# Performance work log

Measured on AMD Instinct MI355X. Metric: run time of the kernel, lower is better.

The kernel has to match this reference:

```python
import jax, jax.numpy as jnp
import numpy as np

NUM_HEADS, NUM_KEYS, NUM_VALUES, NUM_OUTPUTS = 8, 64, 64, 512
B, H, W, C = 16, 64, 64, 512


def setup_inputs() -> dict:
    key = jax.random.key(0)
    ks = jax.random.split(key, 5)
    def xavier(k, shape):
        fan_in, fan_out = shape
        lim = np.sqrt(6.0 / (fan_in + fan_out))
        return jax.random.uniform(k, shape, jnp.float32, -lim, lim)
    return {
        "x": jax.random.normal(ks[0], (B, H, W, C), jnp.float32),
        "Wq": xavier(ks[1], (C, NUM_HEADS * NUM_KEYS)),
        "bq": jnp.zeros((NUM_HEADS * NUM_KEYS,), jnp.float32),
        "Wk": xavier(ks[2], (C, NUM_HEADS * NUM_KEYS)),
        "bk": jnp.zeros((NUM_HEADS * NUM_KEYS,), jnp.float32),
        "Wv": xavier(ks[3], (C, NUM_HEADS * NUM_VALUES)),
        "bv": jnp.zeros((NUM_HEADS * NUM_VALUES,), jnp.float32),
        "Wo": xavier(ks[4], (NUM_VALUES, NUM_OUTPUTS)),
        "bo": jnp.zeros((NUM_OUTPUTS,), jnp.float32),
    }


def reference(x, Wq, bq, Wk, bk, Wv, bv, Wo, bo):
    b, h, w, c = x.shape
    n, dk, dv = NUM_HEADS, NUM_KEYS, NUM_VALUES
    # single pooled query per image
    q = (jnp.mean(x, axis=(1, 2)) @ Wq + bq).reshape(b, n, dk)      # [B,N,dk]
    K = (x @ Wk + bk).reshape(b, h, w, n, dk)                        # [B,H,W,N,dk]
    V = (x @ Wv + bv).reshape(b, h, w, n, dv)                        # [B,H,W,N,dv]
    scale = 1.0 / jnp.sqrt(jnp.float32(dk))
    # scores of the single query against every pixel
    s = jnp.einsum('bnk,bhwnk->bnhw', q, K) * scale                  # [B,N,H,W]
    attn_h = jax.nn.softmax(s, axis=-1)   # per row, softmax over width
    attn_v = jax.nn.softmax(s, axis=-2)   # per column, softmax over height
    A_h = jnp.einsum('bnhw,bhwnv->bnhv', attn_h, V)                  # [B,N,H,dv]
    A_v = jnp.einsum('bnhw,bhwnv->bnwv', attn_v, V)                  # [B,N,W,dv]
    # outer-product combine over spatial dims, summed over heads
    A = jnp.einsum('bnhv,bnwv->bhwv', A_h, A_v)                      # [B,H,W,dv]
    return A @ Wo + bo                                               # [B,H,W,num_outputs]
```

## Files before the change

### kernel.cpp

```cpp
#include <hip/hip_runtime.h>
#include <hip/hip_bf16.h>

#define NHEADS 8
#define DK 64
#define DV 64
#define CIN 512
#define PIX_PER_IMG 4096
#define NPIX 65536

typedef short bf16x8 __attribute__((ext_vector_type(8)));
typedef float f32x4 __attribute__((ext_vector_type(4)));

__device__ __forceinline__ float b2f(unsigned int u) {
  union { unsigned int i; float f; } v; v.i = u << 16; return v.f;
}
__device__ __forceinline__ unsigned short f2b(float f) {
  union { float f; unsigned int i; } v; v.f = f;
  unsigned int x = v.i;
  return (unsigned short)((x + 0x7fffu + ((x >> 16) & 1u)) >> 16);
}
__device__ __forceinline__ void gload_lds16(const void* g, void* l) {
  __builtin_amdgcn_global_load_lds(
      (const __attribute__((address_space(1))) void*)g,
      (__attribute__((address_space(3))) void*)l, 16, 0, 0);
}

__global__ __launch_bounds__(256) void k_pool_prep(
    const float* __restrict__ x, unsigned short* __restrict__ xb,
    float* __restrict__ partial,
    const float* __restrict__ Wv, const float* __restrict__ Wo,
    unsigned short* __restrict__ WvT, unsigned short* __restrict__ WoT) {
  int blk = blockIdx.x;
  int t = threadIdx.x;
  if (blk >= 2048) {
    int idx = (blk - 2048) * 256 + t;
    if (idx < 262144) {
      int n = idx >> 9, c = idx & 511;
      WvT[idx] = f2b(Wv[(size_t)c * 512 + n]);
    } else {
      int j = idx - 262144;
      int o = j >> 6, kk = j & 63;
      WoT[j] = f2b(Wo[(size_t)kk * 512 + o]);
    }
    return;
  }
  int b = blk >> 7, chunk = blk & 127;
  int c4 = t & 127;
  int half = t >> 7;
  size_t rowbase = (size_t)b * PIX_PER_IMG + chunk * 32;
  const float4* x4 = (const float4*)x;
  float4 acc = make_float4(0.f, 0.f, 0.f, 0.f);
#pragma unroll
  for (int i = 0; i < 16; ++i) {
    int p = 2 * i + half;
    float4 v = x4[(rowbase + p) * 128 + c4];
    acc.x += v.x; acc.y += v.y; acc.z += v.z; acc.w += v.w;
    uint2 o;
    o.x = (unsigned)f2b(v.x) | ((unsigned)f2b(v.y) << 16);
    o.y = (unsigned)f2b(v.z) | ((unsigned)f2b(v.w) << 16);
    *(uint2*)(xb + (rowbase + p) * CIN + c4 * 4) = o;
  }
  *(float4*)(partial + ((size_t)(blk * 2 + half)) * CIN + c4 * 4) = acc;
}

__global__ __launch_bounds__(256) void k_qp2(
    const float* __restrict__ partial,
    const float* __restrict__ Wq, const float* __restrict__ bq,
    const float* __restrict__ Wk, float* __restrict__ P) {
  __shared__ float xs[CIN];
  __shared__ float red[256];
  __shared__ float qsh[64];
  int b = blockIdx.x, n = blockIdx.y, t = threadIdx.x;
  for (int c = t; c < CIN; c += 256) {
    float s = 0.f;
    for (int ch = 0; ch < 256; ++ch) s += partial[((size_t)(b * 256 + ch)) * CIN + c];
    xs[c] = s * (1.0f / 4096.0f);
  }
  __syncthreads();
  int jj = t & 63, part = t >> 6;
  {
    float acc = 0.f;
    const float* wp = Wq + (size_t)(part * 128) * CIN + n * 64 + jj;
    for (int ci = 0; ci < 128; ++ci)
      acc += xs[part * 128 + ci] * wp[(size_t)ci * CIN];
    red[t] = acc;
  }
  __syncthreads();
  if (t < 64)
    qsh[t] = red[t] + red[t + 64] + red[t + 128] + red[t + 192] + bq[n * 64 + t];
  __syncthreads();
  for (int c = t; c < CIN; c += 256) {
    float acc = 0.f;
    const float* wr = Wk + (size_t)c * CIN + n * 64;
    for (int k = 0; k < 64; ++k) acc += qsh[k] * wr[k];
    P[((size_t)(b * NHEADS + n)) * CIN + c] = acc;
  }
}

__global__ __launch_bounds__(256) void k_scores(
    const unsigned short* __restrict__ xb, const float* __restrict__ P,
    float* __restrict__ s) {
  __shared__ __align__(16) unsigned short Pl[24 * 520];
  int blk = blockIdx.x;
  int b = blk >> 6, tile = blk & 63;
  int t = threadIdx.x;
  for (int i = t; i < 4096; i += 256) {
    int n = i >> 9, c = i & 511;
    float pv = P[((size_t)(b * NHEADS + n)) * CIN + c];
    unsigned short h = f2b(pv);
    Pl[n * 520 + c] = h;
    Pl[(n + 8) * 520 + c] = f2b(pv - b2f(h));
  }
  __syncthreads();
  int wave = t >> 6, lane = t & 63;
  int prow = lane & 15, kgrp = lane >> 4;
  const unsigned short* arow =
      xb + ((size_t)b * PIX_PER_IMG + tile * 64 + wave * 16 + prow) * CIN + kgrp * 8;
  const unsigned short* bhi = Pl + prow * 520 + kgrp * 8;
  const unsigned short* blo = Pl + (prow + 8) * 520 + kgrp * 8;
  f32x4 acc = (f32x4){0.f, 0.f, 0.f, 0.f};
#pragma unroll
  for (int kb = 0; kb < 16; ++kb) {
    bf16x8 af = *(const bf16x8*)(arow + kb * 32);
    bf16x8 bh = *(const bf16x8*)(bhi + kb * 32);
    bf16x8 bl = *(const bf16x8*)(blo + kb * 32);
    acc = __builtin_amdgcn_mfma_f32_16x16x32_bf16(af, bh, acc, 0, 0, 0);
    acc = __builtin_amdgcn_mfma_f32_16x16x32_bf16(af, bl, acc, 0, 0, 0);
  }
  int n = prow;
  if (n < 8) {
    float* sp = s + ((size_t)(b * NHEADS + n)) * PIX_PER_IMG + tile * 64 + wave * 16 + kgrp * 4;
#pragma unroll
    for (int r = 0; r < 4; ++r) sp[r] = acc[r] * 0.125f;
  }
}

__global__ __launch_bounds__(256) void k_softmax(
    const float* __restrict__ s, float* __restrict__ ah, float* __restrict__ avT) {
  __shared__ float st[4096];
  int bn = blockIdx.x, t = threadIdx.x;
  const float* sp = s + (size_t)bn * 4096;
  for (int i = t; i < 4096; i += 256) st[i] = sp[i];
  __syncthreads();
  int task = t >> 1, half = t & 1;
  int id = task & 63;
  bool isRow = task < 64;
  float v[32];
#pragma unroll
  for (int i = 0; i < 32; ++i) {
    int e = half * 32 + i;
    v[i] = isRow ? st[id * 64 + e] : st[e * 64 + id];
  }
  float m = -1e30f;
#pragma unroll
  for (int i = 0; i < 32; ++i) m = fmaxf(m, v[i]);
  m = fmaxf(m, __shfl_xor(m, 1));
  float sum = 0.f;
#pragma unroll
  for (int i = 0; i < 32; ++i) { v[i] = __expf(v[i] - m); sum += v[i]; }
  sum += __shfl_xor(sum, 1);
  float inv = 1.f / sum;
  float* dst = (isRow ? ah : avT) + (size_t)bn * 4096 + id * 64 + half * 32;
#pragma unroll
  for (int i = 0; i < 32; ++i) dst[i] = v[i] * inv;
}

__global__ __launch_bounds__(256) void k_xhv(
    const unsigned short* __restrict__ xb, const float* __restrict__ ahg,
    const float* __restrict__ avTg, unsigned short* __restrict__ XHV) {
  __shared__ unsigned short xs[64 * 256];
  __shared__ float al[NHEADS * 64];
  int bx = blockIdx.x, ch = blockIdx.y, t = threadIdx.x;
  bool isV = bx >= 1024;
  int bi = isV ? bx - 1024 : bx;
  int b = bi >> 6, rc = bi & 63;
  if (!isV) {
    const unsigned short* src = xb + ((size_t)(b * PIX_PER_IMG + rc * 64)) * CIN + ch * 256;
#pragma unroll
    for (int i = 0; i < 8; ++i) {
      int idx = i * 256 + t;
      int w = idx >> 5, off = idx & 31;
      ((uint4*)xs)[idx] = ((const uint4*)(src + (size_t)w * CIN))[off];
    }
  } else {
#pragma unroll
    for (int i = 0; i < 8; ++i) {
      int idx = i * 256 + t;
      int h = idx >> 5, off = idx & 31;
      ((uint4*)xs)[idx] =
          ((const uint4*)(xb + ((size_t)(b * PIX_PER_IMG + h * 64 + rc)) * CIN + ch * 256))[off];
    }
  }
  const float* ag = isV ? avTg : ahg;
#pragma unroll
  for (int i = 0; i < 2; ++i) {
    int idx = i * 256 + t;
    al[idx] = ag[((size_t)(b * NHEADS + (idx >> 6))) * PIX_PER_IMG + rc * 64 + (idx & 63)];
  }
  __syncthreads();
  int n = t >> 5, oct = t & 31;
  float acc[8] = {0.f, 0.f, 0.f, 0.f, 0.f, 0.f, 0.f, 0.f};
  const float* ar = al + n * 64;
  for (int p = 0; p < 64; ++p) {
    float aw = ar[p];
    uint4 u = *(const uint4*)(xs + (size_t)p * 256 + oct * 8);
    acc[0] += aw * b2f(u.x & 0xffff);
    acc[1] += aw * b2f(u.x >> 16);
    acc[2] += aw * b2f(u.y & 0xffff);
    acc[3] += aw * b2f(u.y >> 16);
    acc[4] += aw * b2f(u.z & 0xffff);
    acc[5] += aw * b2f(u.z >> 16);
    acc[6] += aw * b2f(u.w & 0xffff);
    acc[7] += aw * b2f(u.w >> 16);
  }
  uint4 o;
  o.x = (unsigned)f2b(acc[0]) | ((unsigned)f2b(acc[1]) << 16);
  o.y = (unsigned)f2b(acc[2]) | ((unsigned)f2b(acc[3]) << 16);
  o.z = (unsigned)f2b(acc[4]) | ((unsigned)f2b(acc[5]) << 16);
  o.w = (unsigned)f2b(acc[6]) | ((unsigned)f2b(acc[7]) << 16);
  size_t dst = ((size_t)(n * 2048 + (isV ? 1024 : 0) + b * 64 + rc)) * CIN + ch * 256 + oct * 8;
  *(uint4*)(XHV + dst) = o;
}

__global__ __launch_bounds__(256) void k_gemm2(
    const unsigned short* __restrict__ XHV, const unsigned short* __restrict__ WvT,
    const float* __restrict__ bv, float* __restrict__ Ah, float* __restrict__ Av) {
  __shared__ __align__(16) unsigned short As[128 * 64];
  __shared__ __align__(16) unsigned short Bs[64 * 64];
  const int t = threadIdx.x;
  const int wave = t >> 6, lane = t & 63;
  const int mtile = blockIdx.x, head = blockIdx.y;
  const int m0 = mtile * 128;
  const unsigned short* A = XHV + (size_t)head * 2048 * CIN;
  const unsigned short* BT = WvT + (size_t)head * 64 * CIN;

  f32x4 acc[2][4];
  for (int i = 0; i < 2; ++i)
    for (int j = 0; j < 4; ++j) acc[i][j] = (f32x4){0.f, 0.f, 0.f, 0.f};

  const int lrow = wave * 8 + (lane >> 3);
  const int lcolb = (lane & 7) * 16;

  for (int kt = 0; kt < 8; ++kt) {
    __syncthreads();
#pragma unroll
    for (int j = 0; j < 4; ++j) {
      gload_lds16((const char*)A + ((size_t)(m0 + j * 32 + lrow) * CIN + kt * 64) * 2 + lcolb,
                  (char*)As + (j * 32 + wave * 8) * 128);
    }
#pragma unroll
    for (int j = 0; j < 2; ++j) {
      gload_lds16((const char*)BT + ((size_t)(j * 32 + lrow) * CIN + kt * 64) * 2 + lcolb,
                  (char*)Bs + (j * 32 + wave * 8) * 128);
    }
    __syncthreads();
#pragma unroll
    for (int s = 0; s < 2; ++s) {
      bf16x8 af[2], bg[4];
#pragma unroll
      for (int i = 0; i < 2; ++i) {
        int mrow = wave * 32 + i * 16 + (lane & 15);
        af[i] = *(const bf16x8*)((const char*)As + mrow * 128 + s * 64 + ((lane >> 4) * 16));
      }
#pragma unroll
      for (int j = 0; j < 4; ++j) {
        int nrow = j * 16 + (lane & 15);
        bg[j] = *(const bf16x8*)((const char*)Bs + nrow * 128 + s * 64 + ((lane >> 4) * 16));
      }
#pragma unroll
      for (int i = 0; i < 2; ++i)
#pragma unroll
        for (int j = 0; j < 4; ++j)
          acc[i][j] = __builtin_amdgcn_mfma_f32_16x16x32_bf16(af[i], bg[j], acc[i][j], 0, 0, 0);
    }
  }
#pragma unroll
  for (int i = 0; i < 2; ++i)
#pragma unroll
    for (int j = 0; j < 4; ++j) {
      int v = j * 16 + (lane & 15);
      float bb = bv[head * 64 + v];
#pragma unroll
      for (int r = 0; r < 4; ++r) {
        int m = m0 + wave * 32 + i * 16 + ((lane >> 4) * 4) + r;
        float val = acc[i][j][r] + bb;
        if (m < 1024) {
          int b = m >> 6, h = m & 63;
          Ah[((size_t)(b * NHEADS + head)) * 4096 + h * 64 + v] = val;
        } else {
          int m2 = m - 1024;
          int b = m2 >> 6, w = m2 & 63;
          Av[((size_t)(b * NHEADS + head)) * 4096 + w * 64 + v] = val;
        }
      }
    }
}

__global__ __launch_bounds__(256) void k_outgemm(
    const float* __restrict__ Ah, const float* __restrict__ Av,
    const unsigned short* __restrict__ WoT,
    const float* __restrict__ bo, float* __restrict__ out) {
  __shared__ __align__(16) unsigned short As[128 * 64];
  __shared__ __align__(16) unsigned short Bs[128 * 64];
  const int t = threadIdx.x;
  const int wave = t >> 6, lane = t & 63;
  const int wr = wave >> 1, wc = wave & 1;
  const int m0 = blockIdx.y * 128, n0 = blockIdx.x * 128;
  const int b = m0 >> 12, h0 = (m0 >> 6) & 63;

  const int srow = wave * 32 + (lane >> 3), scolb = (lane & 7) * 16;
#pragma unroll
  for (int j = 0; j < 4; ++j)
    gload_lds16((const char*)WoT + ((size_t)(n0 + srow + j * 8) * 64) * 2 + scolb,
                (char*)Bs + wave * 4096 + j * 1024);

  {
    const int v = t & 63, rg = t >> 6;
    float ahv0[8], ahv1[8];
#pragma unroll
    for (int n = 0; n < 8; ++n) {
      ahv0[n] = Ah[((size_t)((b * 8 + n) * 64 + h0)) * 64 + v];
      ahv1[n] = Ah[((size_t)((b * 8 + n) * 64 + h0 + 1)) * 64 + v];
    }
#pragma unroll 2
    for (int i = 0; i < 16; ++i) {
      int w = rg * 16 + i;
      float a0 = 0.f, a1 = 0.f;
#pragma unroll
      for (int n = 0; n < 8; ++n) {
        float av = Av[((size_t)((b * 8 + n) * 64 + w)) * 64 + v];
        a0 += ahv0[n] * av;
        a1 += ahv1[n] * av;
      }
      As[w * 64 + v] = f2b(a0);
      As[(64 + w) * 64 + v] = f2b(a1);
    }
  }
  __syncthreads();

  f32x4 acc[4][4];
  for (int i = 0; i < 4; ++i)
    for (int j = 0; j < 4; ++j) acc[i][j] = (f32x4){0.f, 0.f, 0.f, 0.f};
#pragma unroll
  for (int s = 0; s < 2; ++s) {
    bf16x8 af[4], bg[4];
#pragma unroll
    for (int i = 0; i < 4; ++i) {
      int mrow = wr * 64 + i * 16 + (lane & 15);
      af[i] = *(const bf16x8*)((const char*)As + mrow * 128 + s * 64 + ((lane >> 4) * 16));
    }
#pragma unroll
    for (int j = 0; j < 4; ++j) {
      int nrow = wc * 64 + j * 16 + (lane & 15);
      bg[j] = *(const bf16x8*)((const char*)Bs + nrow * 128 + s * 64 + ((lane >> 4) * 16));
    }
#pragma unroll
    for (int i = 0; i < 4; ++i)
#pragma unroll
      for (int j = 0; j < 4; ++j)
        acc[i][j] = __builtin_amdgcn_mfma_f32_16x16x32_bf16(af[i], bg[j], acc[i][j], 0, 0, 0);
  }
#pragma unroll
  for (int i = 0; i < 4; ++i)
#pragma unroll
    for (int j = 0; j < 4; ++j) {
      int mbase = m0 + wr * 64 + i * 16 + ((lane >> 4) * 4);
      int n = n0 + wc * 64 + j * 16 + (lane & 15);
      float bb = bo[n];
#pragma unroll
      for (int r = 0; r < 4; ++r)
        out[(size_t)(mbase + r) * 512 + n] = acc[i][j][r] + bb;
    }
}

extern "C" void kernel_launch(void* const* d_in, const int* in_sizes, int n_in,
                              void* d_out, int out_size, void* d_ws, size_t ws_size,
                              hipStream_t stream) {
  (void)in_sizes; (void)n_in; (void)out_size; (void)ws_size;
  const float* x = (const float*)d_in[0];
  const float* Wq = (const float*)d_in[1];
  const float* bq = (const float*)d_in[2];
  const float* Wk = (const float*)d_in[3];
  const float* Wv = (const float*)d_in[5];
  const float* bv = (const float*)d_in[6];
  const float* Wo = (const float*)d_in[7];
  const float* bo = (const float*)d_in[8];
  float* out = (float*)d_out;

  char* ws = (char*)d_ws;
  unsigned short* xb = (unsigned short*)(ws + 0);
  float* partial = (float*)(ws + 67108864);
  float* s = (float*)(ws + 75497472);
  float* P = (float*)(ws + 77594624);
  float* attn_h = (float*)(ws + 77856768);
  float* avT = (float*)(ws + 79953920);
  unsigned short* XHV = (unsigned short*)(ws + 82051072);
  float* Ah = (float*)(ws + 98828288);
  float* Av = (float*)(ws + 100925440);
  unsigned short* WvT = (unsigned short*)(ws + 103022592);
  unsigned short* WoT = (unsigned short*)(ws + 103546880);

  k_pool_prep<<<3200, 256, 0, stream>>>(x, xb, partial, Wv, Wo, WvT, WoT);
  k_qp2<<<dim3(16, 8), 256, 0, stream>>>(partial, Wq, bq, Wk, P);
  k_scores<<<1024, 256, 0, stream>>>(xb, P, s);
  k_softmax<<<128, 256, 0, stream>>>(s, attn_h, avT);
  k_xhv<<<dim3(2048, 2), 256, 0, stream>>>(xb, attn_h, avT, XHV);
  k_gemm2<<<dim3(16, 8), 256, 0, stream>>>(XHV, WvT, bv, Ah, Av);
  k_outgemm<<<dim3(4, 512), 256, 0, stream>>>(Ah, Av, WoT, bo, out);
}
```

Baseline: 369.7 us.

## Fuse softmax into xhv, reduce pool partials in-block, retile gemm2 and outgemm

Removes the separate softmax kernel by computing row/column softmax with wave shuffles inside k_xhv, folding the score scale into P. The pooling kernel now reduces both halves in shared memory so half as many partial sums are written and read in k_qp2. k_gemm2 uses 64-row tiles with twice as many blocks for more parallelism, and k_outgemm handles two N tiles per block, reusing the combined A_h*A_v tile instead of recomputing it. The trade-off is that softmax work is repeated for each of the two channel halves in k_xhv.

```diff
diff --git a/kernel.cpp b/kernel.cpp
--- a/kernel.cpp
+++ b/kernel.cpp
@@ -44,6 +44,7 @@
     }
     return;
   }
+  __shared__ float4 sh[128];
   int b = blk >> 7, chunk = blk & 127;
   int c4 = t & 127;
   int half = t >> 7;
@@ -60,7 +61,13 @@
     o.y = (unsigned)f2b(v.z) | ((unsigned)f2b(v.w) << 16);
     *(uint2*)(xb + (rowbase + p) * CIN + c4 * 4) = o;
   }
-  *(float4*)(partial + ((size_t)(blk * 2 + half)) * CIN + c4 * 4) = acc;
+  if (half) sh[c4] = acc;
+  __syncthreads();
+  if (!half) {
+    float4 o = sh[c4];
+    acc.x += o.x; acc.y += o.y; acc.z += o.z; acc.w += o.w;
+    *(float4*)(partial + (size_t)blk * CIN + c4 * 4) = acc;
+  }
 }
 
 __global__ __launch_bounds__(256) void k_qp2(
@@ -73,7 +80,7 @@
   int b = blockIdx.x, n = blockIdx.y, t = threadIdx.x;
   for (int c = t; c < CIN; c += 256) {
     float s = 0.f;
-    for (int ch = 0; ch < 256; ++ch) s += partial[((size_t)(b * 256 + ch)) * CIN + c];
+    for (int ch = 0; ch < 128; ++ch) s += partial[((size_t)(b * 128 + ch)) * CIN + c];
     xs[c] = s * (1.0f / 4096.0f);
   }
   __syncthreads();
@@ -93,7 +100,7 @@
     float acc = 0.f;
     const float* wr = Wk + (size_t)c * CIN + n * 64;
     for (int k = 0; k < 64; ++k) acc += qsh[k] * wr[k];
-    P[((size_t)(b * NHEADS + n)) * CIN + c] = acc;
+    P[((size_t)(b * NHEADS + n)) * CIN + c] = acc * 0.125f;
   }
 }
 
@@ -131,43 +138,13 @@
   if (n < 8) {
     float* sp = s + ((size_t)(b * NHEADS + n)) * PIX_PER_IMG + tile * 64 + wave * 16 + kgrp * 4;
 #pragma unroll
-    for (int r = 0; r < 4; ++r) sp[r] = acc[r] * 0.125f;
-  }
-}
-
-__global__ __launch_bounds__(256) void k_softmax(
-    const float* __restrict__ s, float* __restrict__ ah, float* __restrict__ avT) {
-  __shared__ float st[4096];
-  int bn = blockIdx.x, t = threadIdx.x;
-  const float* sp = s + (size_t)bn * 4096;
-  for (int i = t; i < 4096; i += 256) st[i] = sp[i];
-  __syncthreads();
-  int task = t >> 1, half = t & 1;
-  int id = task & 63;
-  bool isRow = task < 64;
-  float v[32];
-#pragma unroll
-  for (int i = 0; i < 32; ++i) {
-    int e = half * 32 + i;
-    v[i] = isRow ? st[id * 64 + e] : st[e * 64 + id];
-  }
-  float m = -1e30f;
-#pragma unroll
-  for (int i = 0; i < 32; ++i) m = fmaxf(m, v[i]);
-  m = fmaxf(m, __shfl_xor(m, 1));
-  float sum = 0.f;
-#pragma unroll
-  for (int i = 0; i < 32; ++i) { v[i] = __expf(v[i] - m); sum += v[i]; }
-  sum += __shfl_xor(sum, 1);
-  float inv = 1.f / sum;
-  float* dst = (isRow ? ah : avT) + (size_t)bn * 4096 + id * 64 + half * 32;
-#pragma unroll
-  for (int i = 0; i < 32; ++i) dst[i] = v[i] * inv;
+    for (int r = 0; r < 4; ++r) sp[r] = acc[r];
+  }
 }
 
 __global__ __launch_bounds__(256) void k_xhv(
-    const unsigned short* __restrict__ xb, const float* __restrict__ ahg,
-    const float* __restrict__ avTg, unsigned short* __restrict__ XHV) {
+    const unsigned short* __restrict__ xb, const float* __restrict__ s,
+    unsigned short* __restrict__ XHV) {
   __shared__ unsigned short xs[64 * 256];
   __shared__ float al[NHEADS * 64];
   int bx = blockIdx.x, ch = blockIdx.y, t = threadIdx.x;
@@ -191,11 +168,22 @@
           ((const uint4*)(xb + ((size_t)(b * PIX_PER_IMG + h * 64 + rc)) * CIN + ch * 256))[off];
     }
   }
-  const float* ag = isV ? avTg : ahg;
-#pragma unroll
-  for (int i = 0; i < 2; ++i) {
-    int idx = i * 256 + t;
-    al[idx] = ag[((size_t)(b * NHEADS + (idx >> 6))) * PIX_PER_IMG + rc * 64 + (idx & 63)];
+  {
+    int n = t >> 5, l = t & 31;
+    const float* sp = s + ((size_t)(b * NHEADS + n)) * PIX_PER_IMG;
+    float v0, v1;
+    if (!isV) { v0 = sp[rc * 64 + 2 * l];  v1 = sp[rc * 64 + 2 * l + 1]; }
+    else      { v0 = sp[(2 * l) * 64 + rc]; v1 = sp[(2 * l + 1) * 64 + rc]; }
+    float m = fmaxf(v0, v1);
+#pragma unroll
+    for (int mask = 1; mask <= 16; mask <<= 1) m = fmaxf(m, __shfl_xor(m, mask));
+    float e0 = __expf(v0 - m), e1 = __expf(v1 - m);
+    float sm = e0 + e1;
+#pragma unroll
+    for (int mask = 1; mask <= 16; mask <<= 1) sm += __shfl_xor(sm, mask);
+    float inv = 1.f / sm;
+    al[n * 64 + 2 * l] = e0 * inv;
+    al[n * 64 + 2 * l + 1] = e1 * inv;
   }
   __syncthreads();
   int n = t >> 5, oct = t & 31;
@@ -225,18 +213,16 @@
 __global__ __launch_bounds__(256) void k_gemm2(
     const unsigned short* __restrict__ XHV, const unsigned short* __restrict__ WvT,
     const float* __restrict__ bv, float* __restrict__ Ah, float* __restrict__ Av) {
-  __shared__ __align__(16) unsigned short As[128 * 64];
+  __shared__ __align__(16) unsigned short As[64 * 64];
   __shared__ __align__(16) unsigned short Bs[64 * 64];
   const int t = threadIdx.x;
   const int wave = t >> 6, lane = t & 63;
-  const int mtile = blockIdx.x, head = blockIdx.y;
-  const int m0 = mtile * 128;
+  const int m0 = blockIdx.x * 64, head = blockIdx.y;
   const unsigned short* A = XHV + (size_t)head * 2048 * CIN;
   const unsigned short* BT = WvT + (size_t)head * 64 * CIN;
 
-  f32x4 acc[2][4];
-  for (int i = 0; i < 2; ++i)
-    for (int j = 0; j < 4; ++j) acc[i][j] = (f32x4){0.f, 0.f, 0.f, 0.f};
+  f32x4 acc[4];
+  for (int j = 0; j < 4; ++j) acc[j] = (f32x4){0.f, 0.f, 0.f, 0.f};
 
   const int lrow = wave * 8 + (lane >> 3);
   const int lcolb = (lane & 7) * 16;
@@ -244,56 +230,46 @@
   for (int kt = 0; kt < 8; ++kt) {
     __syncthreads();
 #pragma unroll
-    for (int j = 0; j < 4; ++j) {
+    for (int j = 0; j < 2; ++j)
       gload_lds16((const char*)A + ((size_t)(m0 + j * 32 + lrow) * CIN + kt * 64) * 2 + lcolb,
                   (char*)As + (j * 32 + wave * 8) * 128);
-    }
-#pragma unroll
-    for (int j = 0; j < 2; ++j) {
+#pragma unroll
+    for (int j = 0; j < 2; ++j)
       gload_lds16((const char*)BT + ((size_t)(j * 32 + lrow) * CIN + kt * 64) * 2 + lcolb,
                   (char*)Bs + (j * 32 + wave * 8) * 128);
-    }
     __syncthreads();
 #pragma unroll
-    for (int s = 0; s < 2; ++s) {
-      bf16x8 af[2], bg[4];
-#pragma unroll
-      for (int i = 0; i < 2; ++i) {
-        int mrow = wave * 32 + i * 16 + (lane & 15);
-        af[i] = *(const bf16x8*)((const char*)As + mrow * 128 + s * 64 + ((lane >> 4) * 16));
-      }
-#pragma unroll
-      for (int j = 0; j < 4; ++j) {
-        int nrow = j * 16 + (lane & 15);
-        bg[j] = *(const bf16x8*)((const char*)Bs + nrow * 128 + s * 64 + ((lane >> 4) * 16));
-      }
-#pragma unroll
-      for (int i = 0; i < 2; ++i)
-#pragma unroll
-        for (int j = 0; j < 4; ++j)
-          acc[i][j] = __builtin_amdgcn_mfma_f32_16x16x32_bf16(af[i], bg[j], acc[i][j], 0, 0, 0);
-    }
-  }
-#pragma unroll
-  for (int i = 0; i < 2; ++i)
-#pragma unroll
-    for (int j = 0; j < 4; ++j) {
-      int v = j * 16 + (lane & 15);
-      float bb = bv[head * 64 + v];
-#pragma unroll
-      for (int r = 0; r < 4; ++r) {
-        int m = m0 + wave * 32 + i * 16 + ((lane >> 4) * 4) + r;
-        float val = acc[i][j][r] + bb;
-        if (m < 1024) {
-          int b = m >> 6, h = m & 63;
-          Ah[((size_t)(b * NHEADS + head)) * 4096 + h * 64 + v] = val;
-        } else {
-          int m2 = m - 1024;
-          int b = m2 >> 6, w = m2 & 63;
-          Av[((size_t)(b * NHEADS + head)) * 4096 + w * 64 + v] = val;
-        }
-      }
-    }
+    for (int ss = 0; ss < 2; ++ss) {
+      bf16x8 af = *(const bf16x8*)((const char*)As + (wave * 16 + (lane & 15)) * 128 +
+                                   ss * 64 + ((lane >> 4) * 16));
+      bf16x8 bg[4];
+#pragma unroll
+      for (int j = 0; j < 4; ++j)
+        bg[j] = *(const bf16x8*)((const char*)Bs + (j * 16 + (lane & 15)) * 128 +
+                                 ss * 64 + ((lane >> 4) * 16));
+#pragma unroll
+      for (int j = 0; j < 4; ++j)
+        acc[j] = __builtin_amdgcn_mfma_f32_16x16x32_bf16(af, bg[j], acc[j], 0, 0, 0);
+    }
+  }
+#pragma unroll
+  for (int j = 0; j < 4; ++j) {
+    int v = j * 16 + (lane & 15);
+    float bb = bv[head * 64 + v];
+#pragma unroll
+    for (int r = 0; r < 4; ++r) {
+      int m = m0 + wave * 16 + ((lane >> 4) * 4) + r;
+      float val = acc[j][r] + bb;
+      if (m < 1024) {
+        int b = m >> 6, h = m & 63;
+        Ah[((size_t)(b * NHEADS + head)) * 4096 + h * 64 + v] = val;
+      } else {
+        int m2 = m - 1024;
+        int b = m2 >> 6, w = m2 & 63;
+        Av[((size_t)(b * NHEADS + head)) * 4096 + w * 64 + v] = val;
+      }
+    }
+  }
 }
 
 __global__ __launch_bounds__(256) void k_outgemm(
@@ -305,15 +281,17 @@
   const int t = threadIdx.x;
   const int wave = t >> 6, lane = t & 63;
   const int wr = wave >> 1, wc = wave & 1;
-  const int m0 = blockIdx.y * 128, n0 = blockIdx.x * 128;
+  const int m0 = blockIdx.y * 128;
   const int b = m0 >> 12, h0 = (m0 >> 6) & 63;
 
   const int srow = wave * 32 + (lane >> 3), scolb = (lane & 7) * 16;
-#pragma unroll
-  for (int j = 0; j < 4; ++j)
-    gload_lds16((const char*)WoT + ((size_t)(n0 + srow + j * 8) * 64) * 2 + scolb,
-                (char*)Bs + wave * 4096 + j * 1024);
-
+  {
+    int n0 = blockIdx.x * 256;
+#pragma unroll
+    for (int j = 0; j < 4; ++j)
+      gload_lds16((const char*)WoT + ((size_t)(n0 + srow + j * 8) * 64) * 2 + scolb,
+                  (char*)Bs + wave * 4096 + j * 1024);
+  }
   {
     const int v = t & 63, rg = t >> 6;
     float ahv0[8], ahv1[8];
@@ -336,41 +314,52 @@
       As[(64 + w) * 64 + v] = f2b(a1);
     }
   }
-  __syncthreads();
-
-  f32x4 acc[4][4];
-  for (int i = 0; i < 4; ++i)
-    for (int j = 0; j < 4; ++j) acc[i][j] = (f32x4){0.f, 0.f, 0.f, 0.f};
-#pragma unroll
-  for (int s = 0; s < 2; ++s) {
-    bf16x8 af[4], bg[4];
-#pragma unroll
-    for (int i = 0; i < 4; ++i) {
-      int mrow = wr * 64 + i * 16 + (lane & 15);
-      af[i] = *(const bf16x8*)((const char*)As + mrow * 128 + s * 64 + ((lane >> 4) * 16));
-    }
-#pragma unroll
-    for (int j = 0; j < 4; ++j) {
-      int nrow = wc * 64 + j * 16 + (lane & 15);
-      bg[j] = *(const bf16x8*)((const char*)Bs + nrow * 128 + s * 64 + ((lane >> 4) * 16));
-    }
-#pragma unroll
+
+  for (int nt = 0; nt < 2; ++nt) {
+    const int n0 = (blockIdx.x * 2 + nt) * 128;
+    if (nt) {
+      __syncthreads();
+#pragma unroll
+      for (int j = 0; j < 4; ++j)
+        gload_lds16((const char*)WoT + ((size_t)(n0 + srow + j * 8) * 64) * 2 + scolb,
+                    (char*)Bs + wave * 4096 + j * 1024);
+    }
+    __syncthreads();
+
+    f32x4 acc[4][4];
     for (int i = 0; i < 4; ++i)
-#pragma unroll
-      for (int j = 0; j < 4; ++j)
-        acc[i][j] = __builtin_amdgcn_mfma_f32_16x16x32_bf16(af[i], bg[j], acc[i][j], 0, 0, 0);
-  }
-#pragma unroll
-  for (int i = 0; i < 4; ++i)
-#pragma unroll
-    for (int j = 0; j < 4; ++j) {
-      int mbase = m0 + wr * 64 + i * 16 + ((lane >> 4) * 4);
-      int n = n0 + wc * 64 + j * 16 + (lane & 15);
-      float bb = bo[n];
-#pragma unroll
-      for (int r = 0; r < 4; ++r)
-        out[(size_t)(mbase + r) * 512 + n] = acc[i][j][r] + bb;
-    }
+      for (int j = 0; j < 4; ++j) acc[i][j] = (f32x4){0.f, 0.f, 0.f, 0.f};
+#pragma unroll
+    for (int ss = 0; ss < 2; ++ss) {
+      bf16x8 af[4], bg[4];
+#pragma unroll
+      for (int i = 0; i < 4; ++i) {
+        int mrow = wr * 64 + i * 16 + (lane & 15);
+        af[i] = *(const bf16x8*)((const char*)As + mrow * 128 + ss * 64 + ((lane >> 4) * 16));
+      }
+#pragma unroll
+      for (int j = 0; j < 4; ++j) {
+        int nrow = wc * 64 + j * 16 + (lane & 15);
+        bg[j] = *(const bf16x8*)((const char*)Bs + nrow * 128 + ss * 64 + ((lane >> 4) * 16));
+      }
+#pragma unroll
+      for (int i = 0; i < 4; ++i)
+#pragma unroll
+        for (int j = 0; j < 4; ++j)
+          acc[i][j] = __builtin_amdgcn_mfma_f32_16x16x32_bf16(af[i], bg[j], acc[i][j], 0, 0, 0);
+    }
+#pragma unroll
+    for (int i = 0; i < 4; ++i)
+#pragma unroll
+      for (int j = 0; j < 4; ++j) {
+        int mbase = m0 + wr * 64 + i * 16 + ((lane >> 4) * 4);
+        int n = n0 + wc * 64 + j * 16 + (lane & 15);
+        float bb = bo[n];
+#pragma unroll
+        for (int r = 0; r < 4; ++r)
+          out[(size_t)(mbase + r) * 512 + n] = acc[i][j][r] + bb;
+      }
+  }
 }
 
 extern "C" void kernel_launch(void* const* d_in, const int* in_sizes, int n_in,
@@ -390,21 +379,18 @@
   char* ws = (char*)d_ws;
   unsigned short* xb = (unsigned short*)(ws + 0);
   float* partial = (float*)(ws + 67108864);
-  float* s = (float*)(ws + 75497472);
-  float* P = (float*)(ws + 77594624);
-  float* attn_h = (float*)(ws + 77856768);
-  float* avT = (float*)(ws + 79953920);
-  unsigned short* XHV = (unsigned short*)(ws + 82051072);
-  float* Ah = (float*)(ws + 98828288);
-  float* Av = (float*)(ws + 100925440);
-  unsigned short* WvT = (unsigned short*)(ws + 103022592);
-  unsigned short* WoT = (unsigned short*)(ws + 103546880);
+  float* s = (float*)(ws + 71303168);
+  float* P = (float*)(ws + 73400320);
+  unsigned short* XHV = (unsigned short*)(ws + 73662464);
+  float* Ah = (float*)(ws + 90439680);
+  float* Av = (float*)(ws + 92536832);
+  unsigned short* WvT = (unsigned short*)(ws + 94633984);
+  unsigned short* WoT = (unsigned short*)(ws + 95158272);
 
   k_pool_prep<<<3200, 256, 0, stream>>>(x, xb, partial, Wv, Wo, WvT, WoT);
   k_qp2<<<dim3(16, 8), 256, 0, stream>>>(partial, Wq, bq, Wk, P);
   k_scores<<<1024, 256, 0, stream>>>(xb, P, s);
-  k_softmax<<<128, 256, 0, stream>>>(s, attn_h, avT);
-  k_xhv<<<dim3(2048, 2), 256, 0, stream>>>(xb, attn_h, avT, XHV);
-  k_gemm2<<<dim3(16, 8), 256, 0, stream>>>(XHV, WvT, bv, Ah, Av);
-  k_outgemm<<<dim3(4, 512), 256, 0, stream>>>(Ah, Av, WoT, bo, out);
-}
+  k_xhv<<<dim3(2048, 2), 256, 0, stream>>>(xb, s, XHV);
+  k_gemm2<<<dim3(32, 8), 256, 0, stream>>>(XHV, WvT, bv, Ah, Av);
+  k_outgemm<<<dim3(2, 512), 256, 0, stream>>>(Ah, Av, WoT, bo, out);
+}
```

New measurement: 349.6 us, median of 2. 5.4% less time.
